# Optimization experiments

Measured on AMD Instinct MI355X. Metric: run time of the kernel, lower is better.

## Reference

```python
import jax, jax.numpy as jnp
import numpy as np

NS, NG, E = 4096, 20000, 131072   # samples, genes, edges per relation
DIN, H, C1, C3 = 256, 4, 64, 128  # input dim, heads, layer1 per-head, layer3 per-head


def _gatv2(xs, xd, src, dst, Wl, bl, Wr, br, att, bias, num_dst, out_c, concat):
    """PyG GATv2Conv (add_self_loops=False, no edge_attr), eval mode."""
    xl = (xs @ Wl + bl).reshape(-1, H, out_c)  # [Nsrc,H,C] transformed sources
    xr = (xd @ Wr + br).reshape(-1, H, out_c)  # [Ndst,H,C] transformed targets
    g = jax.nn.leaky_relu(xl[src] + xr[dst], 0.2)          # [E,H,C]
    alpha = jnp.einsum('ehc,hc->eh', g, att)               # [E,H]
    m = jax.ops.segment_max(alpha, dst, num_segments=num_dst)
    ea = jnp.exp(alpha - m[dst])
    den = jax.ops.segment_sum(ea, dst, num_segments=num_dst)
    a = ea / (den[dst] + 1e-16)                            # segment softmax over in-edges
    out = jax.ops.segment_sum(a[:, :, None] * xl[src], dst, num_segments=num_dst)  # [Ndst,H,C]
    out = out.reshape(num_dst, H * out_c) if concat else out.mean(axis=1)
    return out + bias


def setup_inputs() -> dict:
    key = jax.random.key(0)
    ks = jax.random.split(key, 24)
    w = lambda k, s: jax.random.normal(k, s, jnp.float32) * 0.05
    d = {}
    d['x_sample'] = jax.random.normal(ks[0], (NS, DIN), jnp.float32)
    d['x_gene'] = jax.random.normal(ks[1], (NG, DIN), jnp.float32)
    d['sg_src'] = jax.random.randint(ks[2], (E,), 0, NS)
    d['sg_dst'] = jax.random.randint(ks[3], (E,), 0, NG)
    d['gs_src'] = jax.random.randint(ks[4], (E,), 0, NG)
    d['gs_dst'] = jax.random.randint(ks[5], (E,), 0, NS)
    i = 6
    for rel in ('sg', 'gs'):
        d[f'Wl1_{rel}'] = w(ks[i], (DIN, H * C1)); i += 1
        d[f'bl1_{rel}'] = jnp.zeros((H * C1,), jnp.float32)
        d[f'Wr1_{rel}'] = w(ks[i], (DIN, H * C1)); i += 1
        d[f'br1_{rel}'] = jnp.zeros((H * C1,), jnp.float32)
        d[f'att1_{rel}'] = w(ks[i], (H, C1)); i += 1
        d[f'bias1_{rel}'] = jnp.zeros((H * C1,), jnp.float32)
    d['Wl3_gs'] = w(ks[i], (H * C1, H * C3)); i += 1
    d['bl3_gs'] = jnp.zeros((H * C3,), jnp.float32)
    d['Wr3_gs'] = w(ks[i], (H * C1, H * C3)); i += 1
    d['br3_gs'] = jnp.zeros((H * C3,), jnp.float32)
    d['att3_gs'] = w(ks[i], (H, C3)); i += 1
    d['bias3_gs'] = jnp.zeros((C3,), jnp.float32)
    d['sl1_W'] = w(ks[i], (DIN, C1)); i += 1
    d['sl1_b'] = jnp.zeros((C1,), jnp.float32)
    d['sl3_W'] = w(ks[i], (H * C1, C3)); i += 1
    d['sl3_b'] = jnp.zeros((C3,), jnp.float32)
    return d


def reference(x_sample, x_gene, sg_src, sg_dst, gs_src, gs_dst,
              Wl1_sg, bl1_sg, Wr1_sg, br1_sg, att1_sg, bias1_sg,
              Wl1_gs, bl1_gs, Wr1_gs, br1_gs, att1_gs, bias1_gs,
              Wl3_gs, bl3_gs, Wr3_gs, br3_gs, att3_gs, bias3_gs,
              sl1_W, sl1_b, sl3_W, sl3_b):
    # layer 1 (HeteroConv: one GATv2 per relation, concat heads)
    x1_gene = _gatv2(x_sample, x_gene, sg_src, sg_dst,
                     Wl1_sg, bl1_sg, Wr1_sg, br1_sg, att1_sg, bias1_sg, NG, C1, True)
    x1_sample = _gatv2(x_gene, x_sample, gs_src, gs_dst,
                       Wl1_gs, bl1_gs, Wr1_gs, br1_gs, att1_gs, bias1_gs, NS, C1, True)
    # self-loop linear (only for omic/sample nodes), repeated across heads
    x1_sample = x1_sample + jnp.tile(x_sample @ sl1_W + sl1_b, (1, H))
    x1_sample = jax.nn.elu(x1_sample)
    x1_gene = jax.nn.elu(x1_gene)
    # three_layers=False -> x2 = x1; layer 3 (concat=False -> head mean)
    x3_sample = _gatv2(x1_gene, x1_sample, gs_src, gs_dst,
                       Wl3_gs, bl3_gs, Wr3_gs, br3_gs, att3_gs, bias3_gs, NS, C3, False)
    x3_sample = x3_sample + (x1_sample @ sl3_W + sl3_b)
    x3_sample = jax.nn.elu(x3_sample)
    # stack over 1 omic channel -> transpose -> integrator=None -> squeeze
    return x3_sample  # [NS, C3]
```

## Files before the change

kernel.cpp:

```cpp
#include <hip/hip_runtime.h>
#include <hip/hip_bf16.h>
#include <cstdint>

constexpr int kNS = 4096;
constexpr int kNG = 20000;
constexpr int kE  = 131072;
constexpr int kNCAT = kNG + kNS;
constexpr int kNB = (kNCAT + 255) / 256;
constexpr float kL2E = 1.4426950408889634f;

typedef __attribute__((ext_vector_type(8))) short short8;
typedef __attribute__((ext_vector_type(4))) float f32x4;
typedef __attribute__((ext_vector_type(2))) float f32x2;

__device__ __forceinline__ float elu_f(float v) { return v > 0.f ? v : expm1f(v); }

__device__ __forceinline__ unsigned short f2bf(float f) {
  union { float f; unsigned u; } v; v.f = f;
  unsigned r = v.u + 0x7FFF + ((v.u >> 16) & 1);
  return (unsigned short)(r >> 16);
}

__device__ __forceinline__ float bf2f(unsigned short u) {
  union { unsigned u; float f; } v; v.u = ((unsigned)u) << 16; return v.f;
}

__device__ __forceinline__ f32x2 bfp2(unsigned u) {
  union { unsigned u; float f; } lo, hi;
  lo.u = u << 16; hi.u = u & 0xffff0000u;
  return (f32x2){lo.f, hi.f};
}

__global__ __launch_bounds__(256) void zero_int(int* __restrict__ p, int n,
                                                int* __restrict__ padA,
                                                int* __restrict__ padB) {
  int i = blockIdx.x * 256 + threadIdx.x;
  if (i < n) p[i] = 0;
  if (blockIdx.x == 0 && threadIdx.x < 8) {
    padA[threadIdx.x] = 0;
    padB[threadIdx.x] = 0;
  }
}

__global__ __launch_bounds__(256) void prep(
    const float* __restrict__ xs, const float* __restrict__ xg,
    const float* __restrict__ Wl1_sg, const float* __restrict__ Wr1_gs,
    const float* __restrict__ sl1_W, const float* __restrict__ Wr1_sg,
    const float* __restrict__ Wl1_gs, const float* __restrict__ Wl3,
    const float* __restrict__ Wr3, const float* __restrict__ sl3_W,
    const float* __restrict__ bl1_sg, const float* __restrict__ br1_gs,
    const float* __restrict__ sl1_b, const float* __restrict__ br1_sg,
    const float* __restrict__ bl1_gs, const float* __restrict__ br3,
    const float* __restrict__ sl3_b,
    const int* __restrict__ sg_dst, const int* __restrict__ gs_dst,
    int* __restrict__ deg_g, int* __restrict__ deg_s,
    unsigned short* __restrict__ xs_bf, unsigned short* __restrict__ xg_bf,
    unsigned short* __restrict__ Wt1, unsigned short* __restrict__ Wt2,
    unsigned short* __restrict__ Wt3, unsigned short* __restrict__ Wt4,
    float* __restrict__ bc1, float* __restrict__ bc2, float* __restrict__ bc4) {
  __shared__ float tile[64][65];
  int bid = blockIdx.x, tid = threadIdx.x;
  if (bid < 1024) {
    int i = (bid * 256 + tid) * 4;
    float4 v = *(const float4*)&xs[i];
    ushort4 o = {f2bf(v.x), f2bf(v.y), f2bf(v.z), f2bf(v.w)};
    *(ushort4*)&xs_bf[i] = o;
    return;
  }
  bid -= 1024;
  if (bid < 5000) {
    int i = (bid * 256 + tid) * 4;
    float4 v = *(const float4*)&xg[i];
    ushort4 o = {f2bf(v.x), f2bf(v.y), f2bf(v.z), f2bf(v.w)};
    *(ushort4*)&xg_bf[i] = o;
    return;
  }
  bid -= 5000;
  auto wtile = [&](const float* W, unsigned short* Wt, int N, int b) {
    int ntn = N >> 6;
    int tn = b % ntn, tk = b / ntn;
    int c = tid & 63, rb = tid >> 6;
#pragma unroll
    for (int w = 0; w < 16; ++w) {
      int r = rb + w * 4;
      tile[r][c] = W[(size_t)(tk * 64 + r) * N + tn * 64 + c];
    }
    __syncthreads();
#pragma unroll
    for (int w = 0; w < 16; ++w) {
      int n = rb + w * 4;
      Wt[(size_t)(tn * 64 + n) * 256 + tk * 64 + c] = f2bf(tile[c][n]);
    }
  };
  if (bid < 36) {
    int ntn = 9, tn = bid % ntn, tk = bid / ntn;
    int c = tid & 63, rb = tid >> 6;
    int ncol = tn * 64;
#pragma unroll
    for (int w = 0; w < 16; ++w) {
      int r = rb + w * 4;
      int col = ncol + c;
      float v;
      if (col < 256) v = Wl1_sg[(size_t)(tk * 64 + r) * 256 + col];
      else if (col < 512) v = Wr1_gs[(size_t)(tk * 64 + r) * 256 + (col - 256)];
      else v = sl1_W[(size_t)(tk * 64 + r) * 64 + (col - 512)];
      tile[r][c] = v;
    }
    __syncthreads();
#pragma unroll
    for (int w = 0; w < 16; ++w) {
      int n = rb + w * 4;
      Wt1[(size_t)(ncol + n) * 256 + tk * 64 + c] = f2bf(tile[c][n]);
    }
    return;
  }
  bid -= 36;
  if (bid < 32) {
    int ntn = 8, tn = bid % ntn, tk = bid / ntn;
    int c = tid & 63, rb = tid >> 6;
    int ncol = tn * 64;
#pragma unroll
    for (int w = 0; w < 16; ++w) {
      int r = rb + w * 4;
      int col = ncol + c;
      float v = col < 256 ? Wr1_sg[(size_t)(tk * 64 + r) * 256 + col]
                          : Wl1_gs[(size_t)(tk * 64 + r) * 256 + (col - 256)];
      tile[r][c] = v;
    }
    __syncthreads();
#pragma unroll
    for (int w = 0; w < 16; ++w) {
      int n = rb + w * 4;
      Wt2[(size_t)(ncol + n) * 256 + tk * 64 + c] = f2bf(tile[c][n]);
    }
    return;
  }
  bid -= 32;
  if (bid < 32) { wtile(Wl3, Wt3, 512, bid); return; }
  bid -= 32;
  if (bid < 40) {
    int ntn = 10, tn = bid % ntn, tk = bid / ntn;
    int c = tid & 63, rb = tid >> 6;
    int ncol = tn * 64;
#pragma unroll
    for (int w = 0; w < 16; ++w) {
      int r = rb + w * 4;
      int col = ncol + c;
      float v = col < 512 ? Wr3[(size_t)(tk * 64 + r) * 512 + col]
                          : sl3_W[(size_t)(tk * 64 + r) * 128 + (col - 512)];
      tile[r][c] = v;
    }
    __syncthreads();
#pragma unroll
    for (int w = 0; w < 16; ++w) {
      int n = rb + w * 4;
      Wt4[(size_t)(ncol + n) * 256 + tk * 64 + c] = f2bf(tile[c][n]);
    }
    return;
  }
  bid -= 40;
  if (bid < 7) {
    int j = bid * 256 + tid;
    if (j < 256) bc1[j] = bl1_sg[j];
    else if (j < 512) bc1[j] = br1_gs[j - 256];
    else if (j < 576) bc1[j] = sl1_b[j - 512];
    else if (j < 832) bc2[j - 576] = br1_sg[j - 576];
    else if (j < 1088) bc2[j - 576] = bl1_gs[j - 832];
    else if (j < 1600) bc4[j - 1088] = br3[j - 1088];
    else if (j < 1728) bc4[j - 1088] = sl3_b[j - 1600];
    return;
  }
  bid -= 7;
  int i = bid * 256 + tid;
  if (i < kE) atomicAdd(&deg_g[sg_dst[i]], 1);
  else atomicAdd(&deg_s[gs_dst[i - kE]], 1);
}

__global__ __launch_bounds__(256) void scan_fused(
    int* __restrict__ deg, int* __restrict__ rp_g, int* __restrict__ rp_s,
    int* __restrict__ pval, int* __restrict__ pflag) {
  int b = blockIdx.x, t = threadIdx.x;
  int i = b * 256 + t;
  int v = i < kNCAT ? deg[i] : 0;
  __shared__ int s[256];
  s[t] = v;
  __syncthreads();
  for (int ofs = 1; ofs < 256; ofs <<= 1) {
    int add = t >= ofs ? s[t - ofs] : 0;
    __syncthreads();
    s[t] += add;
    __syncthreads();
  }
  if (t == 255) {
    atomicExch(&pval[b], s[255]);
    __threadfence();
    atomicExch(&pflag[b], 1);
  }
  int pre = 0;
  if (t < b) {
    while (atomicAdd(&pflag[t], 0) == 0) {}
    pre = atomicAdd(&pval[t], 0);
  }
  pre += __shfl_xor(pre, 1);  pre += __shfl_xor(pre, 2);
  pre += __shfl_xor(pre, 4);  pre += __shfl_xor(pre, 8);
  pre += __shfl_xor(pre, 16); pre += __shfl_xor(pre, 32);
  __shared__ int ws4[4];
  if ((t & 63) == 0) ws4[t >> 6] = pre;
  __syncthreads();
  int prefix = ws4[0] + ws4[1] + ws4[2] + ws4[3];
  int ex = prefix + s[t] - v;
  if (i < kNG) { rp_g[i] = ex; deg[i] = 0; }
  else if (i < kNCAT) { rp_s[i - kNG] = ex - kE; deg[i] = 0; }
  if (b == 0 && t == 0) { rp_g[kNG] = kE; rp_s[kNS] = kE; }
}

__device__ __forceinline__ void gemm_body(
    const unsigned short* __restrict__ A, const unsigned short* __restrict__ Bt,
    const float* __restrict__ bias, unsigned short* __restrict__ Cb,
    int M, int N, int bx, int by) {
  __shared__ alignas(16) unsigned short As[128 * 32];
  __shared__ alignas(16) unsigned short Bs[64 * 32];
  const int tid = threadIdx.x;
  const int wave = tid >> 6, lane = tid & 63;
  const int brow = by * 128, bcol = bx * 64;
  const int wrow = (wave >> 1) * 64, wcol = (wave & 1) * 32;
  const int la = lane & 15, lk = (lane >> 4) * 8;
  f32x4 acc[4][2] = {};
  for (int k0 = 0; k0 < 256; k0 += 32) {
#pragma unroll
    for (int c = 0; c < 2; ++c) {
      int seg = wave * 128 + c * 64 + lane;
      int row = seg >> 2, ks = (seg & 3) * 8;
      int grow = brow + row; if (grow > M - 1) grow = M - 1;
      const unsigned short* g = A + (size_t)grow * 256 + k0 + ks;
      __builtin_amdgcn_global_load_lds(
          (const __attribute__((address_space(1))) unsigned*)g,
          (__attribute__((address_space(3))) unsigned*)&As[(wave * 128 + c * 64) * 8],
          16, 0, 0);
    }
    {
      int seg = wave * 64 + lane;
      int row = seg >> 2, ks = (seg & 3) * 8;
      const unsigned short* g = Bt + (size_t)(bcol + row) * 256 + k0 + ks;
      __builtin_amdgcn_global_load_lds(
          (const __attribute__((address_space(1))) unsigned*)g,
          (__attribute__((address_space(3))) unsigned*)&Bs[(wave * 64) * 8],
          16, 0, 0);
    }
    __syncthreads();
    short8 bfr[2];
#pragma unroll
    for (int ni = 0; ni < 2; ++ni)
      bfr[ni] = *(const short8*)&Bs[(wcol + ni * 16 + la) * 32 + lk];
#pragma unroll
    for (int mi = 0; mi < 4; ++mi) {
      short8 af = *(const short8*)&As[(wrow + mi * 16 + la) * 32 + lk];
#pragma unroll
      for (int ni = 0; ni < 2; ++ni)
        acc[mi][ni] = __builtin_amdgcn_mfma_f32_16x16x32_bf16(af, bfr[ni], acc[mi][ni], 0, 0, 0);
    }
    __syncthreads();
  }
  const int r0 = (lane >> 4) * 4;
#pragma unroll
  for (int mi = 0; mi < 4; ++mi) {
#pragma unroll
    for (int r = 0; r < 4; ++r) {
      int row = brow + wrow + mi * 16 + r0 + r;
      if (row >= M) continue;
#pragma unroll
      for (int ni = 0; ni < 2; ++ni) {
        int col = bcol + wcol + ni * 16 + la;
        Cb[(size_t)row * N + col] = f2bf(acc[mi][ni][r] + bias[col]);
      }
    }
  }
}

__device__ __forceinline__ void gemm_swz(
    const unsigned short* A, const unsigned short* Bt, const float* bias,
    unsigned short* Cb, int M, int N, int flat, int nbx, int rows_per_xcd) {
  int x = flat & 7, k = flat >> 3;
  int by = x * rows_per_xcd + k / nbx;
  int bx = k % nbx;
  if (by * 128 >= M) return;
  gemm_body(A, Bt, bias, Cb, M, N, bx, by);
}

__global__ __launch_bounds__(256) void gemm_build(
    const unsigned short* __restrict__ A0, const unsigned short* __restrict__ B0,
    const float* __restrict__ b0, unsigned short* __restrict__ C0, int M0, int N0,
    int nb0, int nbx0, int rpx0,
    const unsigned short* __restrict__ A1, const unsigned short* __restrict__ B1,
    const float* __restrict__ b1, unsigned short* __restrict__ C1, int M1, int N1,
    int nb1, int nbx1, int rpx1,
    const int* __restrict__ sgd, const int* __restrict__ sgs,
    const int* __restrict__ rpg, int* __restrict__ curg, int* __restrict__ psg,
    const int* __restrict__ gsd, const int* __restrict__ gss,
    const int* __restrict__ rps, int* __restrict__ curs, int* __restrict__ pss) {
  int flat = blockIdx.x;
  if (flat < nb0) {
    gemm_swz(A0, B0, b0, C0, M0, N0, flat, nbx0, rpx0);
    return;
  }
  flat -= nb0;
  if (flat < nb1) {
    gemm_swz(A1, B1, b1, C1, M1, N1, flat, nbx1, rpx1);
    return;
  }
  flat -= nb1;
  int i = flat * 256 + threadIdx.x;
  if (i < kE) {
    int d = sgd[i];
    psg[rpg[d] + atomicAdd(&curg[d], 1)] = sgs[i] * 576;
  } else {
    i -= kE;
    int d = gsd[i];
    pss[rps[d] + atomicAdd(&curs[d], 1)] = gss[i] * 512;
  }
}

template <bool SPLIT, bool ADDSL>
__device__ __forceinline__ void gat64_body(
    const unsigned short* __restrict__ xl,
    const unsigned short* __restrict__ xr, int ldr,
    const float* __restrict__ att,
    const int* __restrict__ psrc, const int* __restrict__ rp,
    const float* __restrict__ bias,
    const unsigned short* __restrict__ sl, int ldsl,
    unsigned short* __restrict__ out, int N, int rbid) {
  int tid = threadIdx.x;
  int cl = tid & 31;
  int d, sub;
  if (SPLIT) { d = rbid * 4 + (tid >> 6); sub = (tid >> 5) & 1; }
  else       { d = rbid * 8 + (tid >> 5); sub = 0; }
  if (d >= N) return;
  const unsigned short* xlb = xl + cl * 8;
  f32x2 xr2[4], at2[4];
  {
    const uint4 xu = *(const uint4*)&xr[(size_t)d * ldr + cl * 8];
    xr2[0] = bfp2(xu.x); xr2[1] = bfp2(xu.y); xr2[2] = bfp2(xu.z); xr2[3] = bfp2(xu.w);
    float4 a0 = *(const float4*)&att[cl * 8];
    float4 a1 = *(const float4*)&att[cl * 8 + 4];
    at2[0] = (f32x2){a0.x, a0.y} * kL2E; at2[1] = (f32x2){a0.z, a0.w} * kL2E;
    at2[2] = (f32x2){a1.x, a1.y} * kL2E; at2[3] = (f32x2){a1.z, a1.w} * kL2E;
  }
  float l = 0.f;
  f32x2 acc2[4] = {};
  int i0 = rp[d], i1 = rp[d + 1];
  for (int i = SPLIT ? i0 + sub * 4 : i0; i < i1; i += SPLIT ? 8 : 4) {
    int o0 = psrc[i], o1 = psrc[i + 1], o2 = psrc[i + 2], o3 = psrc[i + 3];
    uint4 xu0 = *(const uint4*)&xlb[o0];
    uint4 xu1 = *(const uint4*)&xlb[o1];
    uint4 xu2 = *(const uint4*)&xlb[o2];
    uint4 xu3 = *(const uint4*)&xlb[o3];
    f32x2 xf[4][4];
    xf[0][0] = bfp2(xu0.x); xf[0][1] = bfp2(xu0.y); xf[0][2] = bfp2(xu0.z); xf[0][3] = bfp2(xu0.w);
    xf[1][0] = bfp2(xu1.x); xf[1][1] = bfp2(xu1.y); xf[1][2] = bfp2(xu1.z); xf[1][3] = bfp2(xu1.w);
    xf[2][0] = bfp2(xu2.x); xf[2][1] = bfp2(xu2.y); xf[2][2] = bfp2(xu2.z); xf[2][3] = bfp2(xu2.w);
    xf[3][0] = bfp2(xu3.x); xf[3][1] = bfp2(xu3.y); xf[3][2] = bfp2(xu3.z); xf[3][3] = bfp2(xu3.w);
    float dt[4];
#pragma unroll
    for (int b = 0; b < 4; ++b) {
      f32x2 d2 = {0.f, 0.f};
#pragma unroll
      for (int p = 0; p < 4; ++p) {
        f32x2 v = xf[b][p] + xr2[p];
        f32x2 lk = __builtin_elementwise_max(v, v * 0.2f);
        d2 = __builtin_elementwise_fma(lk, at2[p], d2);
      }
      float dd = d2.x + d2.y;
      dd += __shfl_xor(dd, 1);
      dd += __shfl_xor(dd, 2);
      dd += __shfl_xor(dd, 4);
      dt[b] = dd;
    }
    float w0 = __builtin_amdgcn_exp2f(dt[0]);
    float w1 = (i + 1 < i1) ? __builtin_amdgcn_exp2f(dt[1]) : 0.f;
    float w2 = (i + 2 < i1) ? __builtin_amdgcn_exp2f(dt[2]) : 0.f;
    float w3 = (i + 3 < i1) ? __builtin_amdgcn_exp2f(dt[3]) : 0.f;
    l += (w0 + w1) + (w2 + w3);
#pragma unroll
    for (int p = 0; p < 4; ++p) {
      acc2[p] = __builtin_elementwise_fma(xf[0][p], (f32x2){w0, w0}, acc2[p]);
      acc2[p] = __builtin_elementwise_fma(xf[1][p], (f32x2){w1, w1}, acc2[p]);
      acc2[p] = __builtin_elementwise_fma(xf[2][p], (f32x2){w2, w2}, acc2[p]);
      acc2[p] = __builtin_elementwise_fma(xf[3][p], (f32x2){w3, w3}, acc2[p]);
    }
  }
  if (SPLIT) {
    l += __shfl_xor(l, 32);
#pragma unroll
    for (int p = 0; p < 4; ++p) {
      acc2[p].x += __shfl_xor(acc2[p].x, 32);
      acc2[p].y += __shfl_xor(acc2[p].y, 32);
    }
    if (sub != 0) return;
  }
  float dinv = __builtin_amdgcn_rcpf(l + 1e-16f);
  short8 o;
#pragma unroll
  for (int p = 0; p < 4; ++p) {
    int c = cl * 8 + p * 2;
    float v0 = acc2[p].x * dinv + bias[c];
    float v1 = acc2[p].y * dinv + bias[c + 1];
    if (ADDSL) {
      v0 += bf2f(sl[(size_t)d * ldsl + (c & 63)]);
      v1 += bf2f(sl[(size_t)d * ldsl + ((c + 1) & 63)]);
    }
    o[p * 2]     = (short)f2bf(elu_f(v0));
    o[p * 2 + 1] = (short)f2bf(elu_f(v1));
  }
  *(short8*)&out[(size_t)d * 256 + cl * 8] = o;
}

__global__ __launch_bounds__(256) void gat12(
    const unsigned short* __restrict__ xlA,
    const unsigned short* __restrict__ xrA, int ldrA,
    const float* __restrict__ attA, const int* __restrict__ psA,
    const int* __restrict__ rpA, const float* __restrict__ biasA,
    unsigned short* __restrict__ outA, int NA, int nbA,
    const unsigned short* __restrict__ xlB,
    const unsigned short* __restrict__ xrB, int ldrB,
    const float* __restrict__ attB, const int* __restrict__ psB,
    const int* __restrict__ rpB, const float* __restrict__ biasB,
    const unsigned short* __restrict__ slB, int ldslB,
    unsigned short* __restrict__ outB, int NB) {
  int bid = blockIdx.x;
  if (bid < nbA)
    gat64_body<false, false>(xlA, xrA, ldrA, attA, psA, rpA, biasA,
                             nullptr, 0, outA, NA, bid);
  else
    gat64_body<true, true>(xlB, xrB, ldrB, attB, psB, rpB, biasB,
                           slB, ldslB, outB, NB, bid - nbA);
}

__global__ __launch_bounds__(256) void gat3(
    const unsigned short* __restrict__ xl,
    const unsigned short* __restrict__ xr,
    const float* __restrict__ att,
    const int* __restrict__ psrc, const int* __restrict__ rp,
    const float* __restrict__ bias,
    const unsigned short* __restrict__ sl,
    float* __restrict__ out) {
  __shared__ float sm_acc[2][64][8];
  __shared__ float sm_l[2][64];
  int w = threadIdx.x >> 6, lane = threadIdx.x & 63;
  int p = w >> 1, wp = w & 1;
  int d = blockIdx.x * 2 + p;
  const unsigned short* xlb = xl + lane * 8;
  f32x2 xr2[4], at2[4];
  {
    const uint4 xu = *(const uint4*)&xr[(size_t)d * 640 + lane * 8];
    xr2[0] = bfp2(xu.x); xr2[1] = bfp2(xu.y); xr2[2] = bfp2(xu.z); xr2[3] = bfp2(xu.w);
    float4 a0 = *(const float4*)&att[lane * 8];
    float4 a1 = *(const float4*)&att[lane * 8 + 4];
    at2[0] = (f32x2){a0.x, a0.y} * kL2E; at2[1] = (f32x2){a0.z, a0.w} * kL2E;
    at2[2] = (f32x2){a1.x, a1.y} * kL2E; at2[3] = (f32x2){a1.z, a1.w} * kL2E;
  }
  float l = 0.f;
  f32x2 acc2[4] = {};
  int i0 = rp[d], i1 = rp[d + 1];
  for (int i = i0 + wp * 4; i < i1; i += 8) {
    int o0 = psrc[i], o1 = psrc[i + 1], o2 = psrc[i + 2], o3 = psrc[i + 3];
    uint4 xu0 = *(const uint4*)&xlb[o0];
    uint4 xu1 = *(const uint4*)&xlb[o1];
    uint4 xu2 = *(const uint4*)&xlb[o2];
    uint4 xu3 = *(const uint4*)&xlb[o3];
    f32x2 xf[4][4];
    xf[0][0] = bfp2(xu0.x); xf[0][1] = bfp2(xu0.y); xf[0][2] = bfp2(xu0.z); xf[0][3] = bfp2(xu0.w);
    xf[1][0] = bfp2(xu1.x); xf[1][1] = bfp2(xu1.y); xf[1][2] = bfp2(xu1.z); xf[1][3] = bfp2(xu1.w);
    xf[2][0] = bfp2(xu2.x); xf[2][1] = bfp2(xu2.y); xf[2][2] = bfp2(xu2.z); xf[2][3] = bfp2(xu2.w);
    xf[3][0] = bfp2(xu3.x); xf[3][1] = bfp2(xu3.y); xf[3][2] = bfp2(xu3.z); xf[3][3] = bfp2(xu3.w);
    float dt[4];
#pragma unroll
    for (int b = 0; b < 4; ++b) {
      f32x2 d2 = {0.f, 0.f};
#pragma unroll
      for (int q = 0; q < 4; ++q) {
        f32x2 v = xf[b][q] + xr2[q];
        f32x2 lk = __builtin_elementwise_max(v, v * 0.2f);
        d2 = __builtin_elementwise_fma(lk, at2[q], d2);
      }
      float dd = d2.x + d2.y;
      dd += __shfl_xor(dd, 1);
      dd += __shfl_xor(dd, 2);
      dd += __shfl_xor(dd, 4);
      dd += __shfl_xor(dd, 8);
      dt[b] = dd;
    }
    float w0 = __builtin_amdgcn_exp2f(dt[0]);
    float w1 = (i + 1 < i1) ? __builtin_amdgcn_exp2f(dt[1]) : 0.f;
    float w2 = (i + 2 < i1) ? __builtin_amdgcn_exp2f(dt[2]) : 0.f;
    float w3 = (i + 3 < i1) ? __builtin_amdgcn_exp2f(dt[3]) : 0.f;
    l += (w0 + w1) + (w2 + w3);
#pragma unroll
    for (int q = 0; q < 4; ++q) {
      acc2[q] = __builtin_elementwise_fma(xf[0][q], (f32x2){w0, w0}, acc2[q]);
      acc2[q] = __builtin_elementwise_fma(xf[1][q], (f32x2){w1, w1}, acc2[q]);
      acc2[q] = __builtin_elementwise_fma(xf[2][q], (f32x2){w2, w2}, acc2[q]);
      acc2[q] = __builtin_elementwise_fma(xf[3][q], (f32x2){w3, w3}, acc2[q]);
    }
  }
  if (wp == 1) {
#pragma unroll
    for (int q = 0; q < 4; ++q) {
      sm_acc[p][lane][q * 2]     = acc2[q].x;
      sm_acc[p][lane][q * 2 + 1] = acc2[q].y;
    }
    sm_l[p][lane] = l;
  }
  __syncthreads();
  if (wp == 0) {
    l += sm_l[p][lane];
    float dinv = __builtin_amdgcn_rcpf(l + 1e-16f);
    float r[8];
#pragma unroll
    for (int q = 0; q < 4; ++q) {
      r[q * 2]     = (acc2[q].x + sm_acc[p][lane][q * 2]) * dinv;
      r[q * 2 + 1] = (acc2[q].y + sm_acc[p][lane][q * 2 + 1]) * dinv;
    }
#pragma unroll
    for (int j = 0; j < 8; ++j) {
      r[j] += __shfl_xor(r[j], 16);
      r[j] += __shfl_xor(r[j], 32);
    }
    if (lane < 16) {
#pragma unroll
      for (int j = 0; j < 8; ++j) {
        int c = lane * 8 + j;
        out[(size_t)d * 128 + c] =
            elu_f(0.25f * r[j] + bias[c] + bf2f(sl[(size_t)d * 640 + c]));
      }
    }
  }
}

extern "C" void kernel_launch(void* const* d_in, const int* in_sizes, int n_in,
                              void* d_out, int out_size, void* d_ws, size_t ws_size,
                              hipStream_t stream) {
  const float* x_sample = (const float*)d_in[0];
  const float* x_gene   = (const float*)d_in[1];
  const int* sg_src = (const int*)d_in[2];
  const int* sg_dst = (const int*)d_in[3];
  const int* gs_src = (const int*)d_in[4];
  const int* gs_dst = (const int*)d_in[5];
  const float* Wl1_sg = (const float*)d_in[6];
  const float* bl1_sg = (const float*)d_in[7];
  const float* Wr1_sg = (const float*)d_in[8];
  const float* br1_sg = (const float*)d_in[9];
  const float* att1_sg = (const float*)d_in[10];
  const float* bias1_sg = (const float*)d_in[11];
  const float* Wl1_gs = (const float*)d_in[12];
  const float* bl1_gs = (const float*)d_in[13];
  const float* Wr1_gs = (const float*)d_in[14];
  const float* br1_gs = (const float*)d_in[15];
  const float* att1_gs = (const float*)d_in[16];
  const float* bias1_gs = (const float*)d_in[17];
  const float* Wl3 = (const float*)d_in[18];
  const float* bl3 = (const float*)d_in[19];
  const float* Wr3 = (const float*)d_in[20];
  const float* br3 = (const float*)d_in[21];
  const float* att3 = (const float*)d_in[22];
  const float* bias3 = (const float*)d_in[23];
  const float* sl1_W = (const float*)d_in[24];
  const float* sl1_b = (const float*)d_in[25];
  const float* sl3_W = (const float*)d_in[26];
  const float* sl3_b = (const float*)d_in[27];

  float* ws = (float*)d_ws;
  size_t off = 0;
  auto alloc = [&](size_t n) { float* p = ws + off; off += n; return p; };
  float* bc1 = alloc(576);
  float* bc2 = alloc(512);
  float* bc4 = alloc(640);
  unsigned short* cat1 = (unsigned short*)alloc((size_t)kNS * 576 / 2);
  unsigned short* cat2 = (unsigned short*)alloc((size_t)kNG * 512 / 2);
  unsigned short* xl3  = (unsigned short*)alloc((size_t)kNG * 512 / 2);
  unsigned short* cat4 = (unsigned short*)alloc((size_t)kNS * 640 / 2);
  unsigned short* xs_bf  = (unsigned short*)alloc((size_t)kNS * 256 / 2);
  unsigned short* xg_bf  = (unsigned short*)alloc((size_t)kNG * 256 / 2);
  unsigned short* xg1_bf = (unsigned short*)alloc((size_t)kNG * 256 / 2);
  unsigned short* xs1_bf = (unsigned short*)alloc((size_t)kNS * 256 / 2);
  unsigned short* Wt1 = (unsigned short*)alloc(576 * 256 / 2);
  unsigned short* Wt2 = (unsigned short*)alloc(512 * 256 / 2);
  unsigned short* Wt3 = (unsigned short*)alloc(512 * 256 / 2);
  unsigned short* Wt4 = (unsigned short*)alloc(640 * 256 / 2);
  int* deg_g  = (int*)alloc(kNG);
  int* deg_s  = (int*)alloc(kNS);
  int* pval   = (int*)alloc(128);
  int* pflag  = (int*)alloc(128);
  int* rp_g   = (int*)alloc(kNG + 1);
  int* rp_s   = (int*)alloc(kNS + 1);
  int* psrc_g = (int*)alloc(kE + 8);
  int* psrc_s = (int*)alloc(kE + 8);

  zero_int<<<(kNCAT + 256 + 255) / 256, 256, 0, stream>>>(
      deg_g, kNCAT + 256, psrc_g + kE, psrc_s + kE);

  prep<<<7195, 256, 0, stream>>>(
      x_sample, x_gene, Wl1_sg, Wr1_gs, sl1_W, Wr1_sg, Wl1_gs, Wl3, Wr3, sl3_W,
      bl1_sg, br1_gs, sl1_b, br1_sg, bl1_gs, br3, sl3_b,
      sg_dst, gs_dst, deg_g, deg_s,
      xs_bf, xg_bf, Wt1, Wt2, Wt3, Wt4, bc1, bc2, bc4);

  scan_fused<<<kNB, 256, 0, stream>>>(deg_g, rp_g, rp_s, pval, pflag);

  gemm_build<<<288 + 1280 + 1024, 256, 0, stream>>>(
      xs_bf, Wt1, bc1, cat1, kNS, 576, 288, 9, 4,
      xg_bf, Wt2, bc2, cat2, kNG, 512, 1280, 8, 20,
      sg_dst, sg_src, rp_g, deg_g, psrc_g,
      gs_dst, gs_src, rp_s, deg_s, psrc_s);

  gat12<<<2500 + 1024, 256, 0, stream>>>(
      cat1, cat2, 512, att1_sg, psrc_g, rp_g, bias1_sg, xg1_bf, kNG, 2500,
      cat2 + 256, cat1 + 256, 576, att1_gs, psrc_s, rp_s, bias1_gs,
      cat1 + 512, 576, xs1_bf, kNS);

  gemm_build<<<1280 + 320, 256, 0, stream>>>(
      xg1_bf, Wt3, bl3, xl3, kNG, 512, 1280, 8, 20,
      xs1_bf, Wt4, bc4, cat4, kNS, 640, 320, 10, 4,
      sg_dst, sg_src, rp_g, deg_g, psrc_g,
      gs_dst, gs_src, rp_s, deg_s, psrc_s);

  gat3<<<kNS / 2, 256, 0, stream>>>(
      xl3, cat4, att3, psrc_s, rp_s, bias3, cat4 + 512, (float*)d_out);
}
```

Before: 149.9 us.

## Gather eight edges per iteration and split gat3 destinations across four waves

The edge loops in the layer-1 and layer-3 GAT kernels now gather eight source rows per iteration instead of four, and convert bf16 values on the fly rather than holding them in a converted array. The goal is more independent gathers in flight to hide memory latency. gat3 now gives each destination its own block, so four waves split the in-edges and their partial results are combined through shared memory. This raises parallelism for the roughly 32-edge sample rows. The cost is more masked-out work on low-degree gene rows and reads of psrc past the end of each row.

New measurement: 157.4 us. 1.05x slower.

```diff
diff --git a/kernel.cpp b/kernel.cpp
--- a/kernel.cpp
+++ b/kernel.cpp
@@ -348,44 +348,42 @@
   float l = 0.f;
   f32x2 acc2[4] = {};
   int i0 = rp[d], i1 = rp[d + 1];
-  for (int i = SPLIT ? i0 + sub * 4 : i0; i < i1; i += SPLIT ? 8 : 4) {
-    int o0 = psrc[i], o1 = psrc[i + 1], o2 = psrc[i + 2], o3 = psrc[i + 3];
-    uint4 xu0 = *(const uint4*)&xlb[o0];
-    uint4 xu1 = *(const uint4*)&xlb[o1];
-    uint4 xu2 = *(const uint4*)&xlb[o2];
-    uint4 xu3 = *(const uint4*)&xlb[o3];
-    f32x2 xf[4][4];
-    xf[0][0] = bfp2(xu0.x); xf[0][1] = bfp2(xu0.y); xf[0][2] = bfp2(xu0.z); xf[0][3] = bfp2(xu0.w);
-    xf[1][0] = bfp2(xu1.x); xf[1][1] = bfp2(xu1.y); xf[1][2] = bfp2(xu1.z); xf[1][3] = bfp2(xu1.w);
-    xf[2][0] = bfp2(xu2.x); xf[2][1] = bfp2(xu2.y); xf[2][2] = bfp2(xu2.z); xf[2][3] = bfp2(xu2.w);
-    xf[3][0] = bfp2(xu3.x); xf[3][1] = bfp2(xu3.y); xf[3][2] = bfp2(xu3.z); xf[3][3] = bfp2(xu3.w);
-    float dt[4];
-#pragma unroll
-    for (int b = 0; b < 4; ++b) {
+  for (int i = SPLIT ? i0 + sub * 8 : i0; i < i1; i += SPLIT ? 16 : 8) {
+    uint4 xu[8];
+#pragma unroll
+    for (int e = 0; e < 8; ++e) xu[e] = *(const uint4*)&xlb[psrc[i + e]];
+    float dt[8];
+#pragma unroll
+    for (int e = 0; e < 8; ++e) {
       f32x2 d2 = {0.f, 0.f};
-#pragma unroll
-      for (int p = 0; p < 4; ++p) {
-        f32x2 v = xf[b][p] + xr2[p];
-        f32x2 lk = __builtin_elementwise_max(v, v * 0.2f);
-        d2 = __builtin_elementwise_fma(lk, at2[p], d2);
-      }
+      f32x2 xv;
+      xv = bfp2(xu[e].x) + xr2[0];
+      d2 = __builtin_elementwise_fma(__builtin_elementwise_max(xv, xv * 0.2f), at2[0], d2);
+      xv = bfp2(xu[e].y) + xr2[1];
+      d2 = __builtin_elementwise_fma(__builtin_elementwise_max(xv, xv * 0.2f), at2[1], d2);
+      xv = bfp2(xu[e].z) + xr2[2];
+      d2 = __builtin_elementwise_fma(__builtin_elementwise_max(xv, xv * 0.2f), at2[2], d2);
+      xv = bfp2(xu[e].w) + xr2[3];
+      d2 = __builtin_elementwise_fma(__builtin_elementwise_max(xv, xv * 0.2f), at2[3], d2);
       float dd = d2.x + d2.y;
       dd += __shfl_xor(dd, 1);
       dd += __shfl_xor(dd, 2);
       dd += __shfl_xor(dd, 4);
-      dt[b] = dd;
-    }
-    float w0 = __builtin_amdgcn_exp2f(dt[0]);
-    float w1 = (i + 1 < i1) ? __builtin_amdgcn_exp2f(dt[1]) : 0.f;
-    float w2 = (i + 2 < i1) ? __builtin_amdgcn_exp2f(dt[2]) : 0.f;
-    float w3 = (i + 3 < i1) ? __builtin_amdgcn_exp2f(dt[3]) : 0.f;
-    l += (w0 + w1) + (w2 + w3);
-#pragma unroll
-    for (int p = 0; p < 4; ++p) {
-      acc2[p] = __builtin_elementwise_fma(xf[0][p], (f32x2){w0, w0}, acc2[p]);
-      acc2[p] = __builtin_elementwise_fma(xf[1][p], (f32x2){w1, w1}, acc2[p]);
-      acc2[p] = __builtin_elementwise_fma(xf[2][p], (f32x2){w2, w2}, acc2[p]);
-      acc2[p] = __builtin_elementwise_fma(xf[3][p], (f32x2){w3, w3}, acc2[p]);
+      dt[e] = dd;
+    }
+    float wgt[8];
+    wgt[0] = __builtin_amdgcn_exp2f(dt[0]);
+#pragma unroll
+    for (int e = 1; e < 8; ++e)
+      wgt[e] = (i + e < i1) ? __builtin_amdgcn_exp2f(dt[e]) : 0.f;
+#pragma unroll
+    for (int e = 0; e < 8; ++e) {
+      l += wgt[e];
+      f32x2 w2 = {wgt[e], wgt[e]};
+      acc2[0] = __builtin_elementwise_fma(bfp2(xu[e].x), w2, acc2[0]);
+      acc2[1] = __builtin_elementwise_fma(bfp2(xu[e].y), w2, acc2[1]);
+      acc2[2] = __builtin_elementwise_fma(bfp2(xu[e].z), w2, acc2[2]);
+      acc2[3] = __builtin_elementwise_fma(bfp2(xu[e].w), w2, acc2[3]);
     }
   }
   if (SPLIT) {
@@ -443,11 +441,10 @@
     const float* __restrict__ bias,
     const unsigned short* __restrict__ sl,
     float* __restrict__ out) {
-  __shared__ float sm_acc[2][64][8];
-  __shared__ float sm_l[2][64];
-  int w = threadIdx.x >> 6, lane = threadIdx.x & 63;
-  int p = w >> 1, wp = w & 1;
-  int d = blockIdx.x * 2 + p;
+  __shared__ float sm_acc[3][64][8];
+  __shared__ float sm_l[3][64];
+  int wp = threadIdx.x >> 6, lane = threadIdx.x & 63;
+  int d = blockIdx.x;
   const unsigned short* xlb = xl + lane * 8;
   f32x2 xr2[4], at2[4];
   {
@@ -461,64 +458,64 @@
   float l = 0.f;
   f32x2 acc2[4] = {};
   int i0 = rp[d], i1 = rp[d + 1];
-  for (int i = i0 + wp * 4; i < i1; i += 8) {
-    int o0 = psrc[i], o1 = psrc[i + 1], o2 = psrc[i + 2], o3 = psrc[i + 3];
-    uint4 xu0 = *(const uint4*)&xlb[o0];
-    uint4 xu1 = *(const uint4*)&xlb[o1];
-    uint4 xu2 = *(const uint4*)&xlb[o2];
-    uint4 xu3 = *(const uint4*)&xlb[o3];
-    f32x2 xf[4][4];
-    xf[0][0] = bfp2(xu0.x); xf[0][1] = bfp2(xu0.y); xf[0][2] = bfp2(xu0.z); xf[0][3] = bfp2(xu0.w);
-    xf[1][0] = bfp2(xu1.x); xf[1][1] = bfp2(xu1.y); xf[1][2] = bfp2(xu1.z); xf[1][3] = bfp2(xu1.w);
-    xf[2][0] = bfp2(xu2.x); xf[2][1] = bfp2(xu2.y); xf[2][2] = bfp2(xu2.z); xf[2][3] = bfp2(xu2.w);
-    xf[3][0] = bfp2(xu3.x); xf[3][1] = bfp2(xu3.y); xf[3][2] = bfp2(xu3.z); xf[3][3] = bfp2(xu3.w);
-    float dt[4];
-#pragma unroll
-    for (int b = 0; b < 4; ++b) {
+  for (int i = i0 + wp * 8; i < i1; i += 32) {
+    uint4 xu[8];
+#pragma unroll
+    for (int e = 0; e < 8; ++e) xu[e] = *(const uint4*)&xlb[psrc[i + e]];
+    float dt[8];
+#pragma unroll
+    for (int e = 0; e < 8; ++e) {
       f32x2 d2 = {0.f, 0.f};
-#pragma unroll
-      for (int q = 0; q < 4; ++q) {
-        f32x2 v = xf[b][q] + xr2[q];
-        f32x2 lk = __builtin_elementwise_max(v, v * 0.2f);
-        d2 = __builtin_elementwise_fma(lk, at2[q], d2);
-      }
+      f32x2 xv;
+      xv = bfp2(xu[e].x) + xr2[0];
+      d2 = __builtin_elementwise_fma(__builtin_elementwise_max(xv, xv * 0.2f), at2[0], d2);
+      xv = bfp2(xu[e].y) + xr2[1];
+      d2 = __builtin_elementwise_fma(__builtin_elementwise_max(xv, xv * 0.2f), at2[1], d2);
+      xv = bfp2(xu[e].z) + xr2[2];
+      d2 = __builtin_elementwise_fma(__builtin_elementwise_max(xv, xv * 0.2f), at2[2], d2);
+      xv = bfp2(xu[e].w) + xr2[3];
+      d2 = __builtin_elementwise_fma(__builtin_elementwise_max(xv, xv * 0.2f), at2[3], d2);
       float dd = d2.x + d2.y;
       dd += __shfl_xor(dd, 1);
       dd += __shfl_xor(dd, 2);
       dd += __shfl_xor(dd, 4);
       dd += __shfl_xor(dd, 8);
-      dt[b] = dd;
-    }
-    float w0 = __builtin_amdgcn_exp2f(dt[0]);
-    float w1 = (i + 1 < i1) ? __builtin_amdgcn_exp2f(dt[1]) : 0.f;
-    float w2 = (i + 2 < i1) ? __builtin_amdgcn_exp2f(dt[2]) : 0.f;
-    float w3 = (i + 3 < i1) ? __builtin_amdgcn_exp2f(dt[3]) : 0.f;
-    l += (w0 + w1) + (w2 + w3);
+      dt[e] = dd;
+    }
+    float wgt[8];
+    wgt[0] = __builtin_amdgcn_exp2f(dt[0]);
+#pragma unroll
+    for (int e = 1; e < 8; ++e)
+      wgt[e] = (i + e < i1) ? __builtin_amdgcn_exp2f(dt[e]) : 0.f;
+#pragma unroll
+    for (int e = 0; e < 8; ++e) {
+      l += wgt[e];
+      f32x2 w2 = {wgt[e], wgt[e]};
+      acc2[0] = __builtin_elementwise_fma(bfp2(xu[e].x), w2, acc2[0]);
+      acc2[1] = __builtin_elementwise_fma(bfp2(xu[e].y), w2, acc2[1]);
+      acc2[2] = __builtin_elementwise_fma(bfp2(xu[e].z), w2, acc2[2]);
+      acc2[3] = __builtin_elementwise_fma(bfp2(xu[e].w), w2, acc2[3]);
+    }
+  }
+  if (wp != 0) {
 #pragma unroll
     for (int q = 0; q < 4; ++q) {
-      acc2[q] = __builtin_elementwise_fma(xf[0][q], (f32x2){w0, w0}, acc2[q]);
-      acc2[q] = __builtin_elementwise_fma(xf[1][q], (f32x2){w1, w1}, acc2[q]);
-      acc2[q] = __builtin_elementwise_fma(xf[2][q], (f32x2){w2, w2}, acc2[q]);
-      acc2[q] = __builtin_elementwise_fma(xf[3][q], (f32x2){w3, w3}, acc2[q]);
-    }
-  }
-  if (wp == 1) {
-#pragma unroll
-    for (int q = 0; q < 4; ++q) {
-      sm_acc[p][lane][q * 2]     = acc2[q].x;
-      sm_acc[p][lane][q * 2 + 1] = acc2[q].y;
-    }
-    sm_l[p][lane] = l;
+      sm_acc[wp - 1][lane][q * 2]     = acc2[q].x;
+      sm_acc[wp - 1][lane][q * 2 + 1] = acc2[q].y;
+    }
+    sm_l[wp - 1][lane] = l;
   }
   __syncthreads();
   if (wp == 0) {
-    l += sm_l[p][lane];
+    l += sm_l[0][lane] + sm_l[1][lane] + sm_l[2][lane];
     float dinv = __builtin_amdgcn_rcpf(l + 1e-16f);
     float r[8];
 #pragma unroll
     for (int q = 0; q < 4; ++q) {
-      r[q * 2]     = (acc2[q].x + sm_acc[p][lane][q * 2]) * dinv;
-      r[q * 2 + 1] = (acc2[q].y + sm_acc[p][lane][q * 2 + 1]) * dinv;
+      r[q * 2] = (acc2[q].x + sm_acc[0][lane][q * 2] + sm_acc[1][lane][q * 2] +
+                  sm_acc[2][lane][q * 2]) * dinv;
+      r[q * 2 + 1] = (acc2[q].y + sm_acc[0][lane][q * 2 + 1] + sm_acc[1][lane][q * 2 + 1] +
+                      sm_acc[2][lane][q * 2 + 1]) * dinv;
     }
 #pragma unroll
     for (int j = 0; j < 8; ++j) {
@@ -623,6 +620,6 @@
       sg_dst, sg_src, rp_g, deg_g, psrc_g,
       gs_dst, gs_src, rp_s, deg_s, psrc_s);
 
-  gat3<<<kNS / 2, 256, 0, stream>>>(
+  gat3<<<kNS, 256, 0, stream>>>(
       xl3, cat4, att3, psrc_s, rp_s, bias3, cat4 + 512, (float*)d_out);
 }
```
